# Kernel optimization log

Measured on AMD Instinct MI355X. Metric: run time of the kernel, lower is better.

The kernel has to match this reference:

```python
import jax, jax.numpy as jnp
import numpy as np
import math

E = 1024   # embed_size
H = 16     # heads arg (actual per-'head' dim due to source's reshape quirk)
G = E // H # 64 head-groups (treated as heads in the source code)
FF = 4 * E


def setup_inputs() -> dict:
    key = jax.random.key(0)
    ks = jax.random.split(key, 12)
    s = 1.0 / math.sqrt(E)
    inp = {
        'x': jax.random.normal(ks[0], (2, 1024, E), dtype=jnp.float32),
        # linear weights stored as (in, out); torch Linear computes x @ W.T + b
        'Wq': jax.random.uniform(ks[1], (E, E), jnp.float32, -s, s),
        'Wk': jax.random.uniform(ks[2], (E, E), jnp.float32, -s, s),
        'Wv': jax.random.uniform(ks[3], (E, E), jnp.float32, -s, s),
        'Wo': jax.random.uniform(ks[4], (E, E), jnp.float32, -s, s),
        'bo': jax.random.uniform(ks[5], (E,), jnp.float32, -s, s),
        'W1': jax.random.uniform(ks[6], (E, FF), jnp.float32, -s, s),
        'b1': jax.random.uniform(ks[7], (FF,), jnp.float32, -s, s),
        'W2': jax.random.uniform(ks[8], (FF, E), jnp.float32, -1.0 / math.sqrt(FF), 1.0 / math.sqrt(FF)),
        'b2': jax.random.uniform(ks[9], (E,), jnp.float32, -s, s),
        'g1': jnp.ones((E,), jnp.float32), 'be1': jnp.zeros((E,), jnp.float32),
        'g2': jnp.ones((E,), jnp.float32), 'be2': jnp.zeros((E,), jnp.float32),
    }
    return inp


def _layernorm(x, g, b, eps=1e-5):
    mu = jnp.mean(x, axis=-1, keepdims=True)
    var = jnp.mean(jnp.square(x - mu), axis=-1, keepdims=True)
    return (x - mu) * jax.lax.rsqrt(var + eps) * g + b


def reference(x, Wq, Wk, Wv, Wo, bo, W1, b1, W2, b2, g1, be1, g2, be2):
    B, S, _ = x.shape
    # QKV projections; faithful to source: split E into (G=E//H groups, H dims),
    # group axis acts as the 'head' axis, per-head dim is H, scale = sqrt(H).
    def split(t):  # [B,S,E] -> [B,G,S,H]
        return t.reshape(B, S, G, H).transpose(0, 2, 1, 3)
    q = split(x @ Wq)
    k = split(x @ Wk)
    v = split(x @ Wv)
    att = jnp.einsum('bgsh,bgth->bgst', q, k) / math.sqrt(H)
    causal = jnp.tril(jnp.ones((S, S), dtype=bool))  # mask==1 above diag -> -inf
    att = jnp.where(causal, att, -jnp.inf)
    att = jax.nn.softmax(att, axis=-1)
    y = jnp.einsum('bgst,bgth->bgsh', att, v)          # [B,G,S,H]
    y = y.transpose(0, 2, 1, 3).reshape(B, S, E)
    attn_out = y @ Wo + bo
    # dropout is identity at inference
    x = _layernorm(attn_out + x, g1, be1)
    ff = jax.nn.relu(x @ W1 + b1) @ W2 + b2
    x = _layernorm(ff + x, g2, be2)
    return x
```

## Files before the change

### kernel.cpp

```cpp
#include <hip/hip_runtime.h>
#include <hip/hip_bf16.h>
#include <math.h>


#define E_DIM 1024
#define S_LEN 1024
#define B_SZ  2
#define G_HEADS 64
#define H_DIM 16
#define FF_DIM 4096
#define M_ROWS (B_SZ * S_LEN)
#define QKV_N  (3 * E_DIM)

#define QSCALE 0.36067376022224085f

#if __has_builtin(__builtin_amdgcn_exp2f)
  #define EXP2(x) __builtin_amdgcn_exp2f(x)
#else
  #define EXP2(x) __expf((x) * 0.6931471805599453f)
#endif

#define VT_STRIDE 136
#define VT_BUF    2312

using bf16x8 = __attribute__((ext_vector_type(8))) short;
using f32x4  = __attribute__((ext_vector_type(4))) float;
using f32x16 = __attribute__((ext_vector_type(16))) float;
using ushort8 = __attribute__((ext_vector_type(8))) unsigned short;

static __device__ __forceinline__ unsigned short f2bf(float f) {
    union { float f; unsigned int u; } x; x.f = f;
    unsigned int r = x.u + 0x7fff + ((x.u >> 16) & 1);
    return (unsigned short)(r >> 16);
}
static __device__ __forceinline__ float bf2f(unsigned short u) {
    union { unsigned int u; float f; } x; x.u = ((unsigned int)u) << 16;
    return x.f;
}
static __device__ __forceinline__ unsigned int pack2(float a, float b) {
    union { __hip_bfloat162 h; unsigned int u; } c;
    c.h = __float22bfloat162_rn(float2{a, b});
    return c.u;
}

__global__ __launch_bounds__(256) void prep_kernel(
    const float* __restrict__ x,
    const float* __restrict__ Wq, const float* __restrict__ Wk,
    const float* __restrict__ Wv, const float* __restrict__ Wo,
    const float* __restrict__ W1_, const float* __restrict__ W2_,
    unsigned short* __restrict__ xb, unsigned short* __restrict__ Wqkt,
    unsigned short* __restrict__ Wot, unsigned short* __restrict__ W1t,
    unsigned short* __restrict__ W2t)
{
    const int id = blockIdx.x;
    if (id < 1024) {
        const size_t i = ((size_t)id * 256 + threadIdx.x) * 8;
        float4 a = *(const float4*)(x + i);
        float4 b = *(const float4*)(x + i + 4);
        ushort8 o;
        o[0] = f2bf(a.x); o[1] = f2bf(a.y); o[2] = f2bf(a.z); o[3] = f2bf(a.w);
        o[4] = f2bf(b.x); o[5] = f2bf(b.y); o[6] = f2bf(b.z); o[7] = f2bf(b.w);
        *(ushort8*)(xb + i) = o;
        return;
    }

    __shared__ float tile[32][33];
    const float* W; unsigned short* Wt; int N, K, n0, k0;
    if (id < 5120) {
        const int q = id - 1024;
        const int z = q >> 10;
        W  = (z == 0) ? Wq : (z == 1) ? Wk : (z == 2) ? Wv : Wo;
        Wt = (z < 3) ? (Wqkt + (size_t)z * E_DIM * E_DIM) : Wot;
        N = E_DIM; K = E_DIM;
        n0 = (q & 31) * 32; k0 = ((q >> 5) & 31) * 32;
    } else {
        const int q = id - 5120;
        const int z = q >> 12;
        const int qx = q & 4095;
        const int bx = qx & 127, by = qx >> 7;
        W  = z ? W2_ : W1_;
        Wt = z ? W2t : W1t;
        N  = z ? E_DIM : FF_DIM;
        K  = z ? FF_DIM : E_DIM;
        n0 = (z ? by : bx) * 32;
        k0 = (z ? bx : by) * 32;
    }
    const int t = threadIdx.x;
    const int r = t >> 3;
    const int c = (t & 7) * 4;

    float4 v = *(const float4*)(W + (size_t)(k0 + r) * N + n0 + c);
    tile[r][c] = v.x; tile[r][c + 1] = v.y; tile[r][c + 2] = v.z; tile[r][c + 3] = v.w;
    __syncthreads();

    ushort4 o;
    o.x = f2bf(tile[c + 0][r]); o.y = f2bf(tile[c + 1][r]);
    o.z = f2bf(tile[c + 2][r]); o.w = f2bf(tile[c + 3][r]);
    *(ushort4*)(Wt + (size_t)(n0 + r) * K + k0 + c) = o;
}

template<int ACT, int OUTBF, int SCALEQ, int NT>
__global__ __launch_bounds__(256) void gemm_mfma(
    const unsigned short* __restrict__ A,
    const unsigned short* __restrict__ Bt,
    const float* __restrict__ bias,
    float* __restrict__ C0, float* __restrict__ C1,
    float* __restrict__ C2, float* __restrict__ C3,
    unsigned short* __restrict__ Cb,
    int Krow, int Kchunk, int ldc)
{
    constexpr int NFR   = NT / 32;
    constexpr int BSUB  = NT * 32;
    constexpr int SUBSZ = 4096 + BSUB;
    __shared__ __align__(16) unsigned short lds[2][2 * SUBSZ];

    const int tid  = threadIdx.x;
    const int wave = tid >> 6;
    const int lane = tid & 63;
    const int wr = wave >> 1;
    const int wc = wave & 1;
    const int row0 = blockIdx.y * 128;
    const int col0 = blockIdx.x * NT;
    const int kbase = blockIdx.z * Kchunk;

    const int lr = lane & 15;
    const int lk = (lane >> 4) * 8;

    const int srow = (lane >> 2);
    const int scol = (lane & 3) * 8;

    f32x4 acc[4][NFR] = {};

    auto STAGE1 = [&](unsigned short* dstA, unsigned short* dstB, int k0) {
        #pragma unroll
        for (int i = 0; i < 2; ++i) {
            const int ci = wave + i * 4;
            const unsigned short* src =
                A + (size_t)(row0 + ci * 16 + srow) * Krow + k0 + scol;
            __builtin_amdgcn_global_load_lds(
                (const __attribute__((address_space(1))) void*)src,
                (__attribute__((address_space(3))) void*)(dstA + ci * 512),
                16, 0, 0);
        }
        #pragma unroll
        for (int i = 0; i < NFR / 2; ++i) {
            const int ci = wave + i * 4;
            const unsigned short* src =
                Bt + (size_t)(col0 + ci * 16 + srow) * Krow + k0 + scol;
            __builtin_amdgcn_global_load_lds(
                (const __attribute__((address_space(1))) void*)src,
                (__attribute__((address_space(3))) void*)(dstB + ci * 512),
                16, 0, 0);
        }
    };
    auto STAGE = [&](int buf, int k0) {
        STAGE1(&lds[buf][0],     &lds[buf][4096],         k0);
        STAGE1(&lds[buf][SUBSZ], &lds[buf][SUBSZ + 4096], k0 + 32);
    };
    auto COMPUTE = [&](int buf, int sub) {
        const unsigned short* As = &lds[buf][sub * SUBSZ];
        const unsigned short* Bs = As + 4096;
        bf16x8 a[4], b[NFR];
        #pragma unroll
        for (int mi = 0; mi < 4; ++mi)
            a[mi] = *(const bf16x8*)(As + (wr * 64 + mi * 16 + lr) * 32 + lk);
        #pragma unroll
        for (int ni = 0; ni < NFR; ++ni)
            b[ni] = *(const bf16x8*)(Bs + (wc * (NT / 2) + ni * 16 + lr) * 32 + lk);
        #pragma unroll
        for (int mi = 0; mi < 4; ++mi)
            #pragma unroll
            for (int ni = 0; ni < NFR; ++ni)
                acc[mi][ni] = __builtin_amdgcn_mfma_f32_16x16x32_bf16(
                    a[mi], b[ni], acc[mi][ni], 0, 0, 0);
    };

    const int nt = Kchunk >> 6;

    STAGE(0, kbase);
    asm volatile("s_waitcnt vmcnt(0)" ::: "memory");
    __builtin_amdgcn_s_barrier();

    int cur = 0;
    for (int t = 0; t < nt; ++t) {
        if (t + 1 < nt) STAGE(cur ^ 1, kbase + (t + 1) * 64);
        COMPUTE(cur, 0);
        COMPUTE(cur, 1);
        asm volatile("s_waitcnt vmcnt(0)" ::: "memory");
        __builtin_amdgcn_s_barrier();
        cur ^= 1;
    }

    const int z = blockIdx.z;
    float* Cw = (z == 0) ? C0 : (z == 1) ? C1 : (z == 2) ? C2 : C3;
    #pragma unroll
    for (int mi = 0; mi < 4; ++mi) {
        #pragma unroll
        for (int ni = 0; ni < NFR; ++ni) {
            const int cc  = col0 + wc * (NT / 2) + ni * 16 + (lane & 15);
            const int rr0 = row0 + wr * 64 + mi * 16 + ((lane >> 4) << 2);
            const float bv = bias ? bias[cc] : 0.f;
            #pragma unroll
            for (int j = 0; j < 4; ++j) {
                float v = acc[mi][ni][j] + bv;
                if (ACT == 1) v = fmaxf(v, 0.f);
                if (SCALEQ && cc < E_DIM) v *= QSCALE;
                if (OUTBF) Cb[(size_t)(rr0 + j) * ldc + cc] = f2bf(v);
                else       Cw[(size_t)(rr0 + j) * ldc + cc] = v;
            }
        }
    }
}

__global__ __launch_bounds__(256) void attn_kernel(
    const unsigned short* __restrict__ qkv, unsigned short* __restrict__ Yb)
{
    __shared__ __align__(16) unsigned short Ks[2][2048];
    __shared__ __align__(16) unsigned short Vt[2][VT_BUF];

    const int bi = blockIdx.x >> 7;
    const int bg = blockIdx.x & 127;
    const int g  = bg & (G_HEADS - 1);
    const int b  = bg >> 6;
    const int tid  = threadIdx.x;
    const int lane = tid & 63;
    const int l31  = lane & 31;
    const int hi   = lane >> 5;
    const int wv   = tid >> 6;
    const int tokb = b * S_LEN;

    const int cblk = 28 - 4 * bi;
    const int q0   = (cblk + wv) * 32;
    const int qrow = q0 + l31;
    const int nt128 = (cblk + 4) >> 2;

    const bf16x8 qf = *(const bf16x8*)(
        qkv + (size_t)(tokb + qrow) * QKV_N + g * H_DIM + hi * 8);

    f32x16 acc = {};
    const f32x16 fz = {};

    const int kv  = tid >> 7;
    const int lw  = (tid >> 6) & 1;
    const int skey0 = lw * 32 + (lane >> 1);
    const int shalf = lane & 1;
    const size_t sgo = (size_t)(g * H_DIM + (1 + kv) * E_DIM + shalf * 8);

    auto STAGE = [&](int buf, int t128, ushort8* vreg) {
        #pragma unroll
        for (int i = 0; i < 2; ++i) {
            const unsigned short* src =
                qkv + (size_t)(tokb + t128 * 128 + skey0 + i * 64) * QKV_N + sgo;
            if (kv == 0) {
                __builtin_amdgcn_global_load_lds(
                    (const __attribute__((address_space(1))) void*)src,
                    (__attribute__((address_space(3))) void*)(
                        &Ks[buf][(lw * 64 + i * 128) * 8]),
                    16, 0, 0);
            } else {
                vreg[i] = *(const ushort8*)src;
            }
        }
    };
    auto WRITE_V = [&](int buf, const ushort8* vreg) {
        if (kv == 1) {
            #pragma unroll
            for (int i = 0; i < 2; ++i)
                #pragma unroll
                for (int j = 0; j < 8; ++j)
                    Vt[buf][(shalf * 8 + j) * VT_STRIDE + skey0 + i * 64] =
                        vreg[i][j];
        }
    };

    const int vrow = (l31 == 16) ? 16 : (l31 & 15);

    auto PROCESS = [&](int cur, int sub, int t0) {
        const bf16x8 kf = *(const bf16x8*)(&Ks[cur][(sub * 32 + l31) * 16 + hi * 8]);
        __builtin_amdgcn_s_setprio(1);
        f32x16 s = __builtin_amdgcn_mfma_f32_32x32x16_bf16(kf, qf, fz, 0, 0, 0);
        __builtin_amdgcn_s_setprio(0);

        float pq[16];
        if (t0 == q0) {
            #pragma unroll
            for (int r = 0; r < 16; ++r) {
                const int key = t0 + (r & 3) + 8 * (r >> 2) + 4 * hi;
                pq[r] = (key > qrow) ? 0.f : EXP2(s[r]);
            }
        } else {
            #pragma unroll
            for (int r = 0; r < 16; ++r) pq[r] = EXP2(s[r]);
        }

        unsigned int cw[8];
        #pragma unroll
        for (int r2 = 0; r2 < 8; ++r2) cw[r2] = pack2(pq[2 * r2], pq[2 * r2 + 1]);

        union { uint4 u; bf16x8 v; } pf0, pf1;
        {
            unsigned int a = cw[0], c = cw[2];
            asm volatile("v_permlane32_swap_b32 %0, %1" : "+v"(a), "+v"(c));
            pf0.u.x = a; pf0.u.z = c;
        }
        {
            unsigned int a = cw[1], c = cw[3];
            asm volatile("v_permlane32_swap_b32 %0, %1" : "+v"(a), "+v"(c));
            pf0.u.y = a; pf0.u.w = c;
        }
        {
            unsigned int a = cw[4], c = cw[6];
            asm volatile("v_permlane32_swap_b32 %0, %1" : "+v"(a), "+v"(c));
            pf1.u.x = a; pf1.u.z = c;
        }
        {
            unsigned int a = cw[5], c = cw[7];
            asm volatile("v_permlane32_swap_b32 %0, %1" : "+v"(a), "+v"(c));
            pf1.u.y = a; pf1.u.w = c;
        }

        const unsigned short* vbase =
            &Vt[cur][vrow * VT_STRIDE + sub * 32 + hi * 8];
        const bf16x8 vb0 = *(const bf16x8*)(vbase);
        const bf16x8 vb1 = *(const bf16x8*)(vbase + 16);

        __builtin_amdgcn_s_setprio(1);
        acc = __builtin_amdgcn_mfma_f32_32x32x16_bf16(pf0.v, vb0, acc, 0, 0, 0);
        acc = __builtin_amdgcn_mfma_f32_32x32x16_bf16(pf1.v, vb1, acc, 0, 0, 0);
        __builtin_amdgcn_s_setprio(0);
    };

    ushort8 vreg[2] = {};
    STAGE(0, 0, vreg);
    if (kv == 1) {
        const int vt = tid - 128;
        Vt[0][16 * VT_STRIDE + vt] = 0x3F80;
        Vt[1][16 * VT_STRIDE + vt] = 0x3F80;
    }
    WRITE_V(0, vreg);
    __syncthreads();

    int cur = 0;
    for (int t = 0; t < nt128; ++t) {
        ushort8 vnext[2] = {};
        const bool more = (t + 1 < nt128);
        if (more) STAGE(cur ^ 1, t + 1, vnext);
        #pragma unroll
        for (int sub = 0; sub < 4; ++sub) {
            const int t0 = t * 128 + sub * 32;
            if (t0 <= q0) PROCESS(cur, sub, t0);
        }
        if (more) WRITE_V(cur ^ 1, vnext);
        asm volatile("s_waitcnt vmcnt(0) lgkmcnt(0)" ::: "memory");
        __builtin_amdgcn_s_barrier();
        cur ^= 1;
    }

    float linv[16];
    #pragma unroll
    for (int r = 0; r < 16; ++r) {
        const float lr_ = __shfl(acc[r], (hi << 5) + 16);
        linv[r] = __builtin_amdgcn_rcpf(lr_);
    }
    if (l31 < H_DIM) {
        #pragma unroll
        for (int r = 0; r < 16; ++r) {
            const int q = (r & 3) + 8 * (r >> 2) + 4 * hi;
            Yb[(size_t)(tokb + q0 + q) * E_DIM + g * H_DIM + l31] =
                f2bf(acc[r] * linv[r]);
        }
    }
}

__global__ __launch_bounds__(256) void add_ln2_kernel(
    const float* __restrict__ P0, const float* __restrict__ P1,
    const float* __restrict__ bias, const float* __restrict__ resid,
    const float* __restrict__ g, const float* __restrict__ be,
    float* __restrict__ O, unsigned short* __restrict__ Ob)
{
    const int row = blockIdx.x;
    const size_t base = (size_t)row * E_DIM;
    const int tid = threadIdx.x;

    float v[4];
    float s = 0.f;
    #pragma unroll
    for (int i = 0; i < 4; ++i) {
        int c = tid + i * 256;
        v[i] = P0[base + c] + P1[base + c] + bias[c] + resid[base + c];
        s += v[i];
    }

    __shared__ float red[256];
    red[tid] = s; __syncthreads();
    for (int st = 128; st >= 1; st >>= 1) {
        if (tid < st) red[tid] += red[tid + st];
        __syncthreads();
    }
    const float mu = red[0] * (1.f / E_DIM);
    __syncthreads();

    float s2 = 0.f;
    #pragma unroll
    for (int i = 0; i < 4; ++i) { float d = v[i] - mu; s2 += d * d; }
    red[tid] = s2; __syncthreads();
    for (int st = 128; st >= 1; st >>= 1) {
        if (tid < st) red[tid] += red[tid + st];
        __syncthreads();
    }
    const float rs = rsqrtf(red[0] * (1.f / E_DIM) + 1e-5f);

    #pragma unroll
    for (int i = 0; i < 4; ++i) {
        int c = tid + i * 256;
        float o = (v[i] - mu) * rs * g[c] + be[c];
        if (O)  O[base + c] = o;
        if (Ob) Ob[base + c] = f2bf(o);
    }
}

__global__ __launch_bounds__(256) void add_ln4_kernel(
    const float* __restrict__ P0, const float* __restrict__ P1,
    const float* __restrict__ P2, const float* __restrict__ P3,
    const float* __restrict__ bias, const unsigned short* __restrict__ residb,
    const float* __restrict__ g, const float* __restrict__ be,
    float* __restrict__ O)
{
    const int row = blockIdx.x;
    const size_t base = (size_t)row * E_DIM;
    const int tid = threadIdx.x;

    float v[4];
    float s = 0.f;
    #pragma unroll
    for (int i = 0; i < 4; ++i) {
        int c = tid + i * 256;
        v[i] = P0[base + c] + P1[base + c] + P2[base + c] + P3[base + c]
             + bias[c] + bf2f(residb[base + c]);
        s += v[i];
    }

    __shared__ float red[256];
    red[tid] = s; __syncthreads();
    for (int st = 128; st >= 1; st >>= 1) {
        if (tid < st) red[tid] += red[tid + st];
        __syncthreads();
    }
    const float mu = red[0] * (1.f / E_DIM);
    __syncthreads();

    float s2 = 0.f;
    #pragma unroll
    for (int i = 0; i < 4; ++i) { float d = v[i] - mu; s2 += d * d; }
    red[tid] = s2; __syncthreads();
    for (int st = 128; st >= 1; st >>= 1) {
        if (tid < st) red[tid] += red[tid + st];
        __syncthreads();
    }
    const float rs = rsqrtf(red[0] * (1.f / E_DIM) + 1e-5f);

    #pragma unroll
    for (int i = 0; i < 4; ++i) {
        int c = tid + i * 256;
        O[base + c] = (v[i] - mu) * rs * g[c] + be[c];
    }
}

extern "C" void kernel_launch(void* const* d_in, const int* in_sizes, int n_in,
                              void* d_out, int out_size, void* d_ws, size_t ws_size,
                              hipStream_t stream)
{
    const float* x  = (const float*)d_in[0];
    const float* Wq = (const float*)d_in[1];
    const float* Wk = (const float*)d_in[2];
    const float* Wv = (const float*)d_in[3];
    const float* Wo = (const float*)d_in[4];
    const float* bo = (const float*)d_in[5];
    const float* W1 = (const float*)d_in[6];
    const float* b1 = (const float*)d_in[7];
    const float* W2 = (const float*)d_in[8];
    const float* b2 = (const float*)d_in[9];
    const float* g1  = (const float*)d_in[10];
    const float* be1 = (const float*)d_in[11];
    const float* g2  = (const float*)d_in[12];
    const float* be2 = (const float*)d_in[13];

    char* W = (char*)d_ws;
    const size_t MB = 1024 * 1024;
    unsigned short* xb   = (unsigned short*)(W + 0 * MB);
    unsigned short* Wqkt = (unsigned short*)(W + 4 * MB);
    unsigned short* qkvb = (unsigned short*)(W + 10 * MB);
    unsigned short* yb   = (unsigned short*)(W + 22 * MB);
    unsigned short* Wot  = (unsigned short*)(W + 26 * MB);
    float* P_o0          = (float*)(W + 4 * MB);
    float* P_o1          = (float*)(W + 12 * MB);
    unsigned short* x1b  = (unsigned short*)(W + 20 * MB);
    unsigned short* W1t  = (unsigned short*)(W + 36 * MB);
    unsigned short* W2t  = (unsigned short*)(W + 44 * MB);
    unsigned short* ff1b = (unsigned short*)(W + 0 * MB);
    float* P_f1          = (float*)(W + 52 * MB);
    float* P_f2          = (float*)(W + 60 * MB);
    float* P_f3          = (float*)(W + 68 * MB);
    float* out           = (float*)d_out;

    dim3 blk(256);

    prep_kernel<<<dim3(13312), blk, 0, stream>>>(
        x, Wq, Wk, Wv, Wo, W1, W2, xb, Wqkt, Wot, W1t, W2t);
    gemm_mfma<0, 1, 1, 128><<<dim3(QKV_N / 128, M_ROWS / 128, 1), blk, 0, stream>>>(
        xb, Wqkt, nullptr, nullptr, nullptr, nullptr, nullptr, qkvb,
        E_DIM, E_DIM, QKV_N);
    attn_kernel<<<dim3(B_SZ * G_HEADS * 8), blk, 0, stream>>>(qkvb, yb);
    gemm_mfma<0, 0, 0, 64><<<dim3(E_DIM / 64, M_ROWS / 128, 2), blk, 0, stream>>>(
        yb, Wot, nullptr, P_o0, P_o1, nullptr, nullptr, nullptr,
        E_DIM, E_DIM / 2, E_DIM);
    add_ln2_kernel<<<dim3(M_ROWS), blk, 0, stream>>>(
        P_o0, P_o1, bo, x, g1, be1, nullptr, x1b);
    gemm_mfma<1, 1, 0, 128><<<dim3(FF_DIM / 128, M_ROWS / 128, 1), blk, 0, stream>>>(
        x1b, W1t, b1, nullptr, nullptr, nullptr, nullptr, ff1b,
        E_DIM, E_DIM, FF_DIM);
    gemm_mfma<0, 0, 0, 128><<<dim3(E_DIM / 128, M_ROWS / 128, 4), blk, 0, stream>>>(
        ff1b, W2t, nullptr, out, P_f1, P_f2, P_f3, nullptr,
        FF_DIM, FF_DIM / 4, E_DIM);
    add_ln4_kernel<<<dim3(M_ROWS), blk, 0, stream>>>(
        out, P_f1, P_f2, P_f3, b2, x1b, g2, be2, out);
}
```

Measured before the change: 143.4 us.

## Use triple-buffered LDS pipeline with partial vmcnt waits in GEMM

Replaces the double-buffered 64-wide K stage (two 32-wide sub-tiles per buffer) with a three-slot ring of 32-wide K stages. Loads run two stages ahead, and each iteration waits only on the oldest outstanding loads via a partial vmcnt count instead of draining all memory traffic. The intent is to overlap global-to-LDS copies with MFMA work more deeply and avoid full stalls each iteration. The cost is one barrier per 32 of K instead of per 64, and the hardcoded vmcnt counts must match the number of loads issued per stage.

```diff
diff --git a/kernel.cpp b/kernel.cpp
--- a/kernel.cpp
+++ b/kernel.cpp
@@ -110,9 +110,8 @@
     int Krow, int Kchunk, int ldc)
 {
     constexpr int NFR   = NT / 32;
-    constexpr int BSUB  = NT * 32;
-    constexpr int SUBSZ = 4096 + BSUB;
-    __shared__ __align__(16) unsigned short lds[2][2 * SUBSZ];
+    constexpr int SUBSZ = 4096 + NT * 32;
+    __shared__ __align__(16) unsigned short lds[3][SUBSZ];
 
     const int tid  = threadIdx.x;
     const int wave = tid >> 6;
@@ -131,7 +130,9 @@
 
     f32x4 acc[4][NFR] = {};
 
-    auto STAGE1 = [&](unsigned short* dstA, unsigned short* dstB, int k0) {
+    auto STAGE = [&](int buf, int k0) {
+        unsigned short* dstA = &lds[buf][0];
+        unsigned short* dstB = &lds[buf][4096];
         #pragma unroll
         for (int i = 0; i < 2; ++i) {
             const int ci = wave + i * 4;
@@ -153,12 +154,8 @@
                 16, 0, 0);
         }
     };
-    auto STAGE = [&](int buf, int k0) {
-        STAGE1(&lds[buf][0],     &lds[buf][4096],         k0);
-        STAGE1(&lds[buf][SUBSZ], &lds[buf][SUBSZ + 4096], k0 + 32);
-    };
-    auto COMPUTE = [&](int buf, int sub) {
-        const unsigned short* As = &lds[buf][sub * SUBSZ];
+    auto COMPUTE = [&](int buf) {
+        const unsigned short* As = &lds[buf][0];
         const unsigned short* Bs = As + 4096;
         bf16x8 a[4], b[NFR];
         #pragma unroll
@@ -175,20 +172,26 @@
                     a[mi], b[ni], acc[mi][ni], 0, 0, 0);
     };
 
-    const int nt = Kchunk >> 6;
+    const int nt = Kchunk >> 5;
 
     STAGE(0, kbase);
-    asm volatile("s_waitcnt vmcnt(0)" ::: "memory");
-    __builtin_amdgcn_s_barrier();
-
-    int cur = 0;
+    STAGE(1, kbase + 32);
+
+    int cur = 0, nxt = 2;
     for (int t = 0; t < nt; ++t) {
-        if (t + 1 < nt) STAGE(cur ^ 1, kbase + (t + 1) * 64);
-        COMPUTE(cur, 0);
-        COMPUTE(cur, 1);
-        asm volatile("s_waitcnt vmcnt(0)" ::: "memory");
+        if (t + 1 < nt) {
+            if constexpr (NT == 128)
+                asm volatile("s_waitcnt vmcnt(4)" ::: "memory");
+            else
+                asm volatile("s_waitcnt vmcnt(3)" ::: "memory");
+        } else {
+            asm volatile("s_waitcnt vmcnt(0)" ::: "memory");
+        }
         __builtin_amdgcn_s_barrier();
-        cur ^= 1;
+        COMPUTE(cur);
+        if (t + 2 < nt) STAGE(nxt, kbase + (t + 2) * 32);
+        cur = (cur == 2) ? 0 : cur + 1;
+        nxt = (nxt == 2) ? 0 : nxt + 1;
     }
 
     const int z = blockIdx.z;
```

Measured after the change: 147.8 us. 3.1% more time.
